# Performance work log

Measured on AMD Instinct MI355X. Metric: run time of the kernel, lower is better.

## Reference

```python
import jax, jax.numpy as jnp
import numpy as np
from jax.scipy.special import logsumexp

B, L, DIN, H, NL, E = 32, 1024, 2048, 1024, 21, 768
LN_EPS = 1e-5

def setup_inputs() -> dict:
    key = jax.random.key(0)
    ks = jax.random.split(key, 8)
    return {
        "seq_feats": jax.random.normal(ks[0], (B, L, DIN), jnp.float32),
        "labels": jax.random.randint(ks[1], (B, L), 0, NL),
        "attention_mask": jnp.ones((B, L), jnp.bool_),
        "W_tok": jax.random.normal(ks[2], (DIN, H), jnp.float32) * 0.02,
        "ln_gamma": jnp.ones((H,), jnp.float32),
        "ln_beta": jnp.zeros((H,), jnp.float32),
        "label_table": jax.random.normal(ks[3], (NL, E), jnp.float32) * 0.02,
        "W_lab": jax.random.normal(ks[4], (E, H), jnp.float32) * 0.02,
        "temperature": jnp.float32(10.0),
        "start_trans": jax.random.uniform(ks[5], (NL,), jnp.float32, -0.1, 0.1),
        "end_trans": jax.random.uniform(ks[6], (NL,), jnp.float32, -0.1, 0.1),
        "trans": jax.random.uniform(ks[7], (NL, NL), jnp.float32, -0.1, 0.1),
    }

def _crf_nll(logits, labels, mask, start_trans, end_trans, trans):
    # torchcrf CRF(batch_first=True), reduction='mean': loss = -mean_b llh_b
    mf = mask.astype(logits.dtype)  # (B,L)
    # --- numerator: score of the gold path ---
    emit = jnp.take_along_axis(logits, labels[..., None], axis=-1)[..., 0]  # (B,L)
    score = start_trans[labels[:, 0]] + emit[:, 0]
    score = score + (emit[:, 1:] * mf[:, 1:]).sum(-1)
    score = score + (trans[labels[:, :-1], labels[:, 1:]] * mf[:, 1:]).sum(-1)
    last_idx = mask.sum(-1).astype(jnp.int32) - 1  # (B,)
    last_tag = jnp.take_along_axis(labels, last_idx[:, None], axis=1)[:, 0]
    score = score + end_trans[last_tag]
    # --- denominator: log partition via forward algorithm (lax.scan over time) ---
    alpha0 = start_trans[None, :] + logits[:, 0]  # (B,NL)
    def step(alpha, xs):
        emit_t, m_t = xs  # (B,NL), (B,)
        new = logsumexp(alpha[:, :, None] + trans[None, :, :] + emit_t[:, None, :], axis=1)
        return jnp.where(m_t[:, None], new, alpha), None
    xs = (jnp.moveaxis(logits[:, 1:], 1, 0), jnp.moveaxis(mask[:, 1:], 1, 0))
    alpha, _ = jax.lax.scan(step, alpha0, xs)
    logZ = logsumexp(alpha + end_trans[None, :], axis=-1)  # (B,)
    return -(score - logZ).mean()

def reference(seq_feats, labels, attention_mask, W_tok, ln_gamma, ln_beta,
              label_table, W_lab, temperature, start_trans, end_trans, trans):
    # token_proj: Linear(no bias) -> LayerNorm -> GELU (exact) -> Dropout(eval=no-op)
    h = seq_feats @ W_tok  # (B,L,H)
    mu = h.mean(-1, keepdims=True)
    var = h.var(-1, keepdims=True)
    h = (h - mu) / jnp.sqrt(var + LN_EPS) * ln_gamma + ln_beta
    token_h = jax.nn.gelu(h, approximate=False)
    label_h = label_table @ W_lab  # (NL,H)
    logits = jnp.einsum('blh,nh->bln', token_h, label_h) * temperature
    loss = _crf_nll(logits, labels, attention_mask, start_trans, end_trans, trans)
    return logits, loss
```

## Files before the change

### kernel.cpp

```cpp
#include <hip/hip_runtime.h>
#include <math.h>

typedef __attribute__((ext_vector_type(8))) short bf16x8;
typedef __attribute__((ext_vector_type(4))) float f32x4;
typedef unsigned short u16;

#define Bsz 32
#define Lsz 1024
#define DIN 2048
#define Hsz 1024
#define NLB 21
#define CCH 64
#define TCH 16

__device__ __forceinline__ float b2f(u16 u) {
  union { unsigned int i; float f; } v; v.i = ((unsigned int)u) << 16; return v.f;
}
__device__ __forceinline__ u16 f2b(float f) {
  union { float f; unsigned int i; } v; v.f = f;
  unsigned int r = v.i + 0x7fffu + ((v.i >> 16) & 1u);
  return (u16)(r >> 16);
}

__global__ void k_convA(const float* __restrict__ in, u16* __restrict__ out, int n4) {
  int idx = blockIdx.x * blockDim.x + threadIdx.x;
  int stride = gridDim.x * blockDim.x;
  const float4* in4 = (const float4*)in;
  ushort4* out4 = (ushort4*)out;
  for (int i = idx; i < n4; i += stride) {
    float4 v = in4[i];
    ushort4 o;
    o.x = f2b(v.x); o.y = f2b(v.y); o.z = f2b(v.z); o.w = f2b(v.w);
    out4[i] = o;
  }
}

__global__ void k_convWT(const float* __restrict__ W, u16* __restrict__ Wt) {
  __shared__ float tile[64][65];
  const int ntile = blockIdx.x & 15;
  const int ktile = blockIdx.x >> 4;
  const int n0 = ntile * 64, k0 = ktile * 64;
  const int tid = threadIdx.x;
#pragma unroll
  for (int i = 0; i < 16; ++i) {
    int lin = i * 256 + tid;
    int r = lin >> 6, c = lin & 63;
    tile[r][c] = W[(size_t)(k0 + r) * Hsz + n0 + c];
  }
  __syncthreads();
#pragma unroll
  for (int i = 0; i < 16; ++i) {
    int lin = i * 256 + tid;
    int r = lin >> 6, c = lin & 63;
    Wt[(size_t)(n0 + r) * DIN + k0 + c] = f2b(tile[c][r]);
  }
}

__global__ void k_trW(const float* __restrict__ WL, float* __restrict__ WLt) {
  __shared__ float tile[64][65];
  const int nt = blockIdx.x & 15;
  const int et = blockIdx.x >> 4;
  const int n0 = nt * 64, e0 = et * 64;
  const int tid = threadIdx.x;
#pragma unroll
  for (int i = 0; i < 16; ++i) {
    int lin = i * 256 + tid;
    int r = lin >> 6, c = lin & 63;
    tile[r][c] = WL[(size_t)(e0 + r) * Hsz + n0 + c];
  }
  __syncthreads();
#pragma unroll
  for (int i = 0; i < 16; ++i) {
    int lin = i * 256 + tid;
    int r = lin >> 6, c = lin & 63;
    WLt[(size_t)(n0 + r) * 768 + e0 + c] = tile[c][r];
  }
}

__global__ __launch_bounds__(256) void k_labelh(const float* __restrict__ LT, const float* __restrict__ WLt,
                                                u16* __restrict__ LH) {
  const int tid = threadIdx.x;
  const int lane = tid & 63;
  const int wave = tid >> 6;
  const int wid = blockIdx.x * 4 + wave;
  const int row = wid >> 10;
  const int col = wid & 1023;
  const float4* a4 = (const float4*)(LT + (size_t)row * 768);
  const float4* b4 = (const float4*)(WLt + (size_t)col * 768);
  float p = 0.f;
#pragma unroll
  for (int it = 0; it < 3; ++it) {
    float4 a = a4[it * 64 + lane];
    float4 b = b4[it * 64 + lane];
    p += a.x * b.x + a.y * b.y + a.z * b.z + a.w * b.w;
  }
#pragma unroll
  for (int o = 32; o; o >>= 1) p += __shfl_xor(p, o);
  if (lane == 0) LH[(size_t)row * Hsz + col] = f2b(p);
}

#define STAGE_A(bufi, h, kt2) do { \
  _Pragma("unroll") \
  for (int it_ = 0; it_ < 2; ++it_) { \
    int row_ = it_ * 128 + (h) * 64 + r0; \
    const u16* s_ = Ab + (size_t)row_ * DIN + (size_t)(kt2) * 64 + cl * 8; \
    __builtin_amdgcn_global_load_lds((const __attribute__((address_space(1))) void*)s_, \
        (__attribute__((address_space(3))) void*)&sA[bufi][row_ * 64 + (tid & 7) * 8], 16, 0, 0); \
  } } while (0)

#define STAGE_B(bufi, h, kt2) do { \
  _Pragma("unroll") \
  for (int it_ = 0; it_ < 2; ++it_) { \
    int row_ = (it_ * 2 + (r0 >> 5)) * 64 + (h) * 32 + (r0 & 31); \
    const u16* s_ = Bb + (size_t)row_ * DIN + (size_t)(kt2) * 64 + cl * 8; \
    __builtin_amdgcn_global_load_lds((const __attribute__((address_space(1))) void*)s_, \
        (__attribute__((address_space(3))) void*)&sB[bufi][row_ * 64 + (tid & 7) * 8], 16, 0, 0); \
  } } while (0)

#define LDA4(dst, sbuf, mh) do { \
  _Pragma("unroll") for (int ks_ = 0; ks_ < 2; ++ks_) \
  _Pragma("unroll") for (int mf_ = 0; mf_ < 4; ++mf_) { \
    int rr_ = wm + (mh) * 64 + mf_ * 16 + (lane & 15); \
    int ck_ = ks_ * 4 + (lane >> 4); \
    dst[mf_][ks_] = *(const bf16x8*)&sA[sbuf][rr_ * 64 + ((ck_ ^ (rr_ & 7)) * 8)]; \
  } } while (0)

#define LDB2(dst, sbuf, nh) do { \
  _Pragma("unroll") for (int ks_ = 0; ks_ < 2; ++ks_) \
  _Pragma("unroll") for (int nf_ = 0; nf_ < 2; ++nf_) { \
    int rr_ = wn + (nh) * 32 + nf_ * 16 + (lane & 15); \
    int ck_ = ks_ * 4 + (lane >> 4); \
    dst[nf_][ks_] = *(const bf16x8*)&sB[sbuf][rr_ * 64 + ((ck_ ^ (rr_ & 7)) * 8)]; \
  } } while (0)

#define MM(aarr, barr, mb, nb) do { \
  __builtin_amdgcn_s_setprio(1); \
  _Pragma("unroll") for (int ks_ = 0; ks_ < 2; ++ks_) \
  _Pragma("unroll") for (int mf_ = 0; mf_ < 4; ++mf_) \
  _Pragma("unroll") for (int nf_ = 0; nf_ < 2; ++nf_) \
    acc[(mb) + mf_][(nb) + nf_] = __builtin_amdgcn_mfma_f32_16x16x32_bf16( \
        aarr[mf_][ks_], barr[nf_][ks_], acc[(mb) + mf_][(nb) + nf_], 0, 0, 0); \
  __builtin_amdgcn_s_setprio(0); \
} while (0)

#define VMC(n)  asm volatile("s_waitcnt vmcnt(" #n ")" ::: "memory")
#define LGKM0() asm volatile("s_waitcnt lgkmcnt(0)" ::: "memory")
#define BARS()  __builtin_amdgcn_s_barrier()

__global__ __launch_bounds__(512, 2) void k_gemm(const u16* __restrict__ A, const u16* __restrict__ Bt,
                                                 u16* __restrict__ H) {
  __shared__ u16 sA[2][256 * 64];
  __shared__ u16 sB[2][256 * 64];
  const int tid = threadIdx.x;
  const int lane = tid & 63;
  const int wave = tid >> 6;
  const int bid = blockIdx.x;
  const int lid = (bid & 7) * 64 + (bid >> 3);
  const int m0 = (lid >> 2) * 256;
  const int n0 = (lid & 3) * 256;
  const int wm = (wave >> 2) * 128;
  const int wn = (wave & 3) * 64;
  const u16* Ab = A + (size_t)m0 * DIN;
  const u16* Bb = Bt + (size_t)n0 * DIN;
  const int r0 = tid >> 3;
  const int cl = (tid & 7) ^ (r0 & 7);

  f32x4 acc[8][4];
#pragma unroll
  for (int i = 0; i < 8; ++i)
#pragma unroll
    for (int j = 0; j < 4; ++j) acc[i][j] = (f32x4){0.f, 0.f, 0.f, 0.f};

  bf16x8 a0[4][2], a1[4][2], b0[2][2], b1[2][2];

  STAGE_A(0, 0, 0); STAGE_B(0, 0, 0); STAGE_A(0, 1, 0); STAGE_B(0, 1, 0);
  STAGE_A(1, 0, 1); STAGE_B(1, 0, 1); STAGE_A(1, 1, 1); STAGE_B(1, 1, 1);
  VMC(8);
  BARS();
  LDA4(a0, 0, 0); LDB2(b0, 0, 0); LDB2(b1, 0, 1);
  LGKM0();
  BARS();

  const int NT = DIN / 64;
  for (int t = 0; t < NT; ++t) {
    const int cur = t & 1, nxt = cur ^ 1;
    MM(a0, b0, 0, 0);
    if (t + 2 < NT) STAGE_A(cur, 0, t + 2);
    if (t < NT - 2)       VMC(12);
    else if (t == NT - 2) VMC(0);
    BARS();
    MM(a0, b1, 0, 2);
    if (t + 2 < NT) STAGE_B(cur, 0, t + 2);
    if (t < NT - 2) VMC(10);
    LDA4(a1, cur, 1);
    LGKM0();
    BARS();
    MM(a1, b1, 4, 2);
    if (t + 2 < NT) STAGE_A(cur, 1, t + 2);
    if (t < NT - 2) VMC(6);
    if (t + 1 < NT) { LDA4(a0, nxt, 0); LGKM0(); }
    BARS();
    MM(a1, b0, 4, 0);
    if (t + 2 < NT) STAGE_B(cur, 1, t + 2);
    if (t + 1 < NT) { LDB2(b0, nxt, 0); LDB2(b1, nxt, 1); LGKM0(); }
    BARS();
  }

#pragma unroll
  for (int mf = 0; mf < 8; ++mf) {
#pragma unroll
    for (int nf = 0; nf < 4; ++nf) {
      int col = n0 + wn + nf * 16 + (lane & 15);
      int er = m0 + wm + mf * 16 + ((lane >> 4) << 2);
#pragma unroll
      for (int r = 0; r < 4; ++r) H[(size_t)(er + r) * Hsz + col] = f2b(acc[mf][nf][r]);
    }
  }
}

__global__ __launch_bounds__(256) void k_head(const u16* __restrict__ Hb, const u16* __restrict__ LH,
                                              const float* __restrict__ gamma, const float* __restrict__ beta,
                                              const float* __restrict__ tempp, float* __restrict__ logits) {
  __shared__ u16 sLH[32 * Hsz];
  const int tid = threadIdx.x;
  const int lane = tid & 63;
  const int wave = tid >> 6;
  for (int id = tid; id < 32 * 64; id += 256) {
    int n = id >> 6, c = id & 63;
    uint4 v = (uint4){0u, 0u, 0u, 0u};
    if (n < NLB) v = *(const uint4*)(LH + (size_t)n * Hsz + c * 8);
    *(uint4*)&sLH[((n << 6) | ((c & 56) | ((c ^ n) & 7))) * 8] = v;
  }
  const float T = tempp[0];
  __syncthreads();

  const int m = lane & 15;
  const int q = lane >> 4;
  const int tok = blockIdx.x * 64 + wave * 16 + m;
  const u16* arow = Hb + (size_t)tok * Hsz;

  float s = 0.f, s2 = 0.f;
  for (int kc = 0; kc < 32; ++kc) {
    bf16x8 v = *(const bf16x8*)(arow + kc * 32 + q * 8);
#pragma unroll
    for (int j = 0; j < 8; ++j) {
      float x = b2f(((const u16*)&v)[j]);
      s += x; s2 += x * x;
    }
  }
  s += __shfl_xor(s, 16);  s += __shfl_xor(s, 32);
  s2 += __shfl_xor(s2, 16); s2 += __shfl_xor(s2, 32);
  const float mu = s * (1.0f / 1024.0f);
  const float rstd = rsqrtf(s2 * (1.0f / 1024.0f) - mu * mu + 1e-5f);

  f32x4 acc0 = (f32x4){0.f, 0.f, 0.f, 0.f};
  f32x4 acc1 = (f32x4){0.f, 0.f, 0.f, 0.f};
  const int nr = lane & 15;
  for (int kc = 0; kc < 32; ++kc) {
    const int k = kc * 32 + q * 8;
    bf16x8 v = *(const bf16x8*)(arow + k);
    float4 g0 = *(const float4*)(gamma + k);
    float4 g1 = *(const float4*)(gamma + k + 4);
    float4 e0 = *(const float4*)(beta + k);
    float4 e1 = *(const float4*)(beta + k + 4);
    float gs[8] = {g0.x, g0.y, g0.z, g0.w, g1.x, g1.y, g1.z, g1.w};
    float bs[8] = {e0.x, e0.y, e0.z, e0.w, e1.x, e1.y, e1.z, e1.w};
    bf16x8 a;
#pragma unroll
    for (int j = 0; j < 8; ++j) {
      float x = b2f(((const u16*)&v)[j]);
      float y = (x - mu) * rstd * gs[j] + bs[j];
      float gl = 0.5f * y * (1.0f + erff(y * 0.70710678118654752f));
      ((u16*)&a)[j] = f2b(gl);
    }
    const int c = kc * 4 + q;
    const int cs = (c & 56) | ((c ^ nr) & 7);
    bf16x8 b0 = *(const bf16x8*)&sLH[((nr << 6) | cs) * 8];
    bf16x8 b1 = *(const bf16x8*)&sLH[(((16 + nr) << 6) | cs) * 8];
    acc0 = __builtin_amdgcn_mfma_f32_16x16x32_bf16(a, b0, acc0, 0, 0, 0);
    acc1 = __builtin_amdgcn_mfma_f32_16x16x32_bf16(a, b1, acc1, 0, 0, 0);
  }
  const int rbase = blockIdx.x * 64 + wave * 16 + q * 4;
#pragma unroll
  for (int r = 0; r < 4; ++r) {
    logits[(size_t)(rbase + r) * NLB + nr] = acc0[r] * T;
    if (nr < 5) logits[(size_t)(rbase + r) * NLB + 16 + nr] = acc1[r] * T;
  }
}

__global__ __launch_bounds__(256) void k_crf1(const float* __restrict__ logits,
                                              const float* __restrict__ trans,
                                              float* __restrict__ Mexp, float* __restrict__ Rlog,
                                              float* __restrict__ loss) {
  __shared__ float sEt[NLB * 24];
  const int tid = threadIdx.x;
  for (int idx = tid; idx < NLB * NLB; idx += 256) {
    int jj = idx / NLB, kk = idx % NLB;
    sEt[jj * 24 + kk] = __expf(trans[kk * NLB + jj]);
  }
  if (blockIdx.x == 0 && tid == 0) *loss = 0.f;
  __syncthreads();

  const int lane = tid & 63;
  const int wave = tid >> 6;
  const int pg = lane >= 42 ? 2 : (lane >= 21 ? 1 : 0);
  const int i0 = lane - pg * 21;
  const bool maskv0 = (lane < 63);
  const int i = i0 > 20 ? 20 : i0;
  const int prob_raw = (blockIdx.x * 4 + wave) * 3 + pg;
  const bool maskv = maskv0 && (prob_raw < Bsz * CCH);
  const int prob = prob_raw < Bsz * CCH ? prob_raw : Bsz * CCH - 1;
  const int b = prob >> 6;
  const int c = prob & 63;
  const int t0 = 1 + c * TCH;
  const float* lg = logits + (size_t)b * Lsz * NLB;

  float P[NLB], rlog = 0.f;
#pragma unroll
  for (int j = 0; j < NLB; ++j)
    P[j] = sEt[j * 24 + i] * __expf(lg[t0 * NLB + j]);
  {
    float m = P[0];
#pragma unroll
    for (int j = 1; j < NLB; ++j) m = fmaxf(m, P[j]);
    rlog = __logf(m);
    float r = 1.0f / m;
#pragma unroll
    for (int j = 0; j < NLB; ++j) P[j] *= r;
  }

  for (int tt = 1; tt < TCH; ++tt) {
    const int t = t0 + tt;
    if (t >= Lsz) break;
    float q[NLB];
#pragma unroll
    for (int j = 0; j < NLB; ++j) {
      const float* e = &sEt[j * 24];
      float4 e0 = *(const float4*)(e);
      float4 e1 = *(const float4*)(e + 4);
      float4 e2 = *(const float4*)(e + 8);
      float4 e3 = *(const float4*)(e + 12);
      float4 e4 = *(const float4*)(e + 16);
      float e5 = e[20];
      float s = P[0] * e0.x + P[1] * e0.y + P[2] * e0.z + P[3] * e0.w
              + P[4] * e1.x + P[5] * e1.y + P[6] * e1.z + P[7] * e1.w
              + P[8] * e2.x + P[9] * e2.y + P[10] * e2.z + P[11] * e2.w
              + P[12] * e3.x + P[13] * e3.y + P[14] * e3.z + P[15] * e3.w
              + P[16] * e4.x + P[17] * e4.y + P[18] * e4.z + P[19] * e4.w
              + P[20] * e5;
      q[j] = s * __expf(lg[t * NLB + j]);
    }
    float m = q[0];
#pragma unroll
    for (int j = 1; j < NLB; ++j) m = fmaxf(m, q[j]);
    rlog += __logf(m);
    float r = 1.0f / m;
#pragma unroll
    for (int j = 0; j < NLB; ++j) P[j] = q[j] * r;
  }

  if (maskv) {
    float* mo = Mexp + ((size_t)prob * NLB + i) * NLB;
#pragma unroll
    for (int j = 0; j < NLB; ++j) mo[j] = P[j];
    Rlog[(size_t)prob * NLB + i] = rlog;
  }
}

__global__ __launch_bounds__(64) void k_crf2(const float* __restrict__ logits, const int* __restrict__ labels,
                                             const float* __restrict__ startt, const float* __restrict__ endt,
                                             const float* __restrict__ trans,
                                             const float* __restrict__ Mexp, const float* __restrict__ Rlog,
                                             float* __restrict__ loss) {
  const int b = blockIdx.x;
  const int lane = threadIdx.x;
  const float* lg = logits + (size_t)b * Lsz * NLB;
  const int* lab = labels + (size_t)b * Lsz;

  float sc = 0.f;
  for (int t = lane; t < Lsz; t += 64) {
    int lt = lab[t];
    sc += lg[t * NLB + lt];
    if (t > 0) sc += trans[lab[t - 1] * NLB + lt];
  }
#pragma unroll
  for (int o = 32; o; o >>= 1) sc += __shfl_xor(sc, o);
  if (lane == 0) sc += startt[lab[0]] + endt[lab[Lsz - 1]];
  const float score = __shfl(sc, 0);

  const bool act = (lane < NLB);
  const int jc = act ? lane : NLB - 1;
  float a0 = act ? (startt[lane] + lg[lane]) : -INFINITY;
  float m = a0;
#pragma unroll
  for (int o = 32; o; o >>= 1) m = fmaxf(m, __shfl_xor(m, o));
  float p = act ? __expf(a0 - m) : 0.f;
  float macc = m;

  for (int c = 0; c < CCH; ++c) {
    const size_t prob = (size_t)b * CCH + c;
    float li = __logf(p) + Rlog[prob * NLB + jc];
    if (!act) li = -INFINITY;
    float S = li;
#pragma unroll
    for (int o = 32; o; o >>= 1) S = fmaxf(S, __shfl_xor(S, o));
    float w = __expf(li - S);
    const float* mc = Mexp + prob * (NLB * NLB) + jc;
    float q0 = 0.f, q1 = 0.f, q2 = 0.f;
#pragma unroll
    for (int ii = 0; ii < NLB; ii += 3) {
      q0 += __shfl(w, ii) * mc[ii * NLB];
      if (ii + 1 < NLB) q1 += __shfl(w, ii + 1) * mc[(ii + 1) * NLB];
      if (ii + 2 < NLB) q2 += __shfl(w, ii + 2) * mc[(ii + 2) * NLB];
    }
    float q = act ? (q0 + q1 + q2) : 0.f;
    float mx = q;
#pragma unroll
    for (int o = 32; o; o >>= 1) mx = fmaxf(mx, __shfl_xor(mx, o));
    p = q * (1.0f / mx);
    macc += S + __logf(mx);
  }

  float z = act ? p * __expf(endt[lane]) : 0.f;
#pragma unroll
  for (int o = 32; o; o >>= 1) z += __shfl_xor(z, o);
  if (lane == 0) {
    float logZ = macc + __logf(z);
    atomicAdd(loss, (logZ - score) * (1.0f / 32.0f));
  }
}

extern "C" void kernel_launch(void* const* d_in, const int* in_sizes, int n_in,
                              void* d_out, int out_size, void* d_ws, size_t ws_size,
                              hipStream_t stream) {
  const float* seq   = (const float*)d_in[0];
  const int*   labs  = (const int*)d_in[1];
  const float* Wtok  = (const float*)d_in[3];
  const float* gamma = (const float*)d_in[4];
  const float* beta  = (const float*)d_in[5];
  const float* LT    = (const float*)d_in[6];
  const float* WL    = (const float*)d_in[7];
  const float* temp  = (const float*)d_in[8];
  const float* st    = (const float*)d_in[9];
  const float* en    = (const float*)d_in[10];
  const float* tr    = (const float*)d_in[11];

  float* logits = (float*)d_out;
  float* loss   = logits + (size_t)Bsz * Lsz * NLB;

  char* ws = (char*)d_ws;
  u16* Abf   = (u16*)(ws);
  u16* Hbf   = (u16*)(ws + 134217728);
  float* WLt = (float*)(ws + 134217728);
  u16* Wt    = (u16*)(ws + 201326592);
  u16* LH    = (u16*)(ws + 205520896);
  float* Mexp = (float*)(ws);
  float* Rlog = (float*)(ws + 3612672);

  k_convA <<<dim3(4096), dim3(256), 0, stream>>>(seq, Abf, (Bsz * Lsz * DIN) / 4);
  k_convWT<<<dim3(512),  dim3(256), 0, stream>>>(Wtok, Wt);
  k_trW   <<<dim3(192),  dim3(256), 0, stream>>>(WL, WLt);
  k_labelh<<<dim3(5376), dim3(256), 0, stream>>>(LT, WLt, LH);
  k_gemm  <<<dim3(512),  dim3(512), 0, stream>>>(Abf, Wt, Hbf);
  k_head  <<<dim3(512),  dim3(256), 0, stream>>>(Hbf, LH, gamma, beta, temp, logits);
  k_crf1  <<<dim3(171),  dim3(256), 0, stream>>>(logits, tr, Mexp, Rlog, loss);
  k_crf2  <<<dim3(32),   dim3(64),  0, stream>>>(logits, labs, st, en, tr, Mexp, Rlog, loss);
}
```

Before: 737.4 us.

## Restructure GEMM main loop to load LDS fragments per quarter step

The bf16 GEMM main loop no longer prefetches the next tile's LDS fragments across iterations. Each iteration now loads its A/B fragments from the current LDS buffer just before the matching MFMA quarter. It uses a partial lgkmcnt wait, adds barriers around each MFMA block, and reorders the global-to-LDS staging of the tile two steps ahead. The likely aim is to cut register pressure and rebalance when staging and MFMAs are issued. The cost is more barriers and less hiding of LDS read latency.

```diff
diff --git a/kernel.cpp b/kernel.cpp
--- a/kernel.cpp
+++ b/kernel.cpp
@@ -144,7 +144,7 @@
 } while (0)
 
 #define VMC(n)  asm volatile("s_waitcnt vmcnt(" #n ")" ::: "memory")
-#define LGKM0() asm volatile("s_waitcnt lgkmcnt(0)" ::: "memory")
+#define LGKMH(n) asm volatile("s_waitcnt lgkmcnt(" #n ")" ::: "memory")
 #define BARS()  __builtin_amdgcn_s_barrier()
 
 __global__ __launch_bounds__(512, 2) void k_gemm(const u16* __restrict__ A, const u16* __restrict__ Bt,
@@ -171,38 +171,38 @@
 #pragma unroll
     for (int j = 0; j < 4; ++j) acc[i][j] = (f32x4){0.f, 0.f, 0.f, 0.f};
 
-  bf16x8 a0[4][2], a1[4][2], b0[2][2], b1[2][2];
-
-  STAGE_A(0, 0, 0); STAGE_B(0, 0, 0); STAGE_A(0, 1, 0); STAGE_B(0, 1, 0);
-  STAGE_A(1, 0, 1); STAGE_B(1, 0, 1); STAGE_A(1, 1, 1); STAGE_B(1, 1, 1);
+  bf16x8 a0f[4][2], a1f[4][2], b0f[2][2], b1f[2][2];
+
+  STAGE_A(0, 0, 0); STAGE_B(0, 0, 0); STAGE_B(0, 1, 0); STAGE_A(0, 1, 0);
+  STAGE_A(1, 0, 1); STAGE_B(1, 0, 1); STAGE_B(1, 1, 1); STAGE_A(1, 1, 1);
   VMC(8);
   BARS();
-  LDA4(a0, 0, 0); LDB2(b0, 0, 0); LDB2(b1, 0, 1);
-  LGKM0();
-  BARS();
 
   const int NT = DIN / 64;
   for (int t = 0; t < NT; ++t) {
-    const int cur = t & 1, nxt = cur ^ 1;
-    MM(a0, b0, 0, 0);
-    if (t + 2 < NT) STAGE_A(cur, 0, t + 2);
-    if (t < NT - 2)       VMC(12);
+    const int cur = t & 1;
+    const bool p2 = (t + 2 < NT);
+    LDA4(a0f, cur, 0);
+    LDB2(b0f, cur, 0);
+    LGKMH(8);
+    BARS();
+    MM(a0f, b0f, 0, 0);
+    BARS();
+    LDB2(b1f, cur, 1);
+    if (p2) STAGE_A(cur, 0, t + 2);
+    BARS();
+    MM(a0f, b1f, 0, 2);
+    BARS();
+    LDA4(a1f, cur, 1);
+    if (p2) STAGE_B(cur, 0, t + 2);
+    BARS();
+    MM(a1f, b0f, 4, 0);
+    BARS();
+    if (p2) { STAGE_B(cur, 1, t + 2); STAGE_A(cur, 1, t + 2); }
+    if (t < NT - 2)       VMC(6);
     else if (t == NT - 2) VMC(0);
     BARS();
-    MM(a0, b1, 0, 2);
-    if (t + 2 < NT) STAGE_B(cur, 0, t + 2);
-    if (t < NT - 2) VMC(10);
-    LDA4(a1, cur, 1);
-    LGKM0();
-    BARS();
-    MM(a1, b1, 4, 2);
-    if (t + 2 < NT) STAGE_A(cur, 1, t + 2);
-    if (t < NT - 2) VMC(6);
-    if (t + 1 < NT) { LDA4(a0, nxt, 0); LGKM0(); }
-    BARS();
-    MM(a1, b0, 4, 0);
-    if (t + 2 < NT) STAGE_B(cur, 1, t + 2);
-    if (t + 1 < NT) { LDB2(b0, nxt, 0); LDB2(b1, nxt, 1); LGKM0(); }
+    MM(a1f, b1f, 4, 2);
     BARS();
   }
 
```

Measured after the change: 725.0 us. About the same (-1.7%).
